# Kernel tuning notes

Hardware: AMD Instinct MI355X
Metric: run time of the kernel (lower is better)

The kernel has to match this reference:

```python
import jax, jax.numpy as jnp
import numpy as np

N_NODES = 50000
N_EDGES = 1600000
NUM_GRAPHS = 64


def gcn_conv(x, edge_index, edge_weight, W, b):
    # PyG GCNConv with normalize=False: h = x @ W; out[i] = sum_{e: tgt(e)=i} w_e * h[src(e)]; out += b
    h = x @ W                                   # [N, out]
    src, tgt = edge_index[0], edge_index[1]
    msg = h[src] * edge_weight[:, None]         # [E, out] gather + scale
    out = jax.ops.segment_sum(msg, tgt, num_segments=N_NODES)
    return out + b


def setup_inputs() -> dict:
    key = jax.random.key(0)
    ks = jax.random.split(key, 10)
    x = jax.random.normal(ks[0], (N_NODES, 128), dtype=jnp.float32)
    edge_index = jax.random.randint(ks[1], (2, N_EDGES), 0, N_NODES, dtype=jnp.int64)
    edge_weight = jax.random.uniform(ks[2], (N_EDGES,), dtype=jnp.float32)
    batch = jnp.sort(jax.random.randint(ks[3], (N_NODES,), 0, NUM_GRAPHS, dtype=jnp.int64))
    W1 = jax.random.normal(ks[4], (128, 64), dtype=jnp.float32) * 0.09  # ~glorot scale
    b1 = jax.random.normal(ks[5], (64,), dtype=jnp.float32) * 0.01
    W2 = jax.random.normal(ks[6], (64, 64), dtype=jnp.float32) * 0.125
    b2 = jax.random.normal(ks[7], (64,), dtype=jnp.float32) * 0.01
    W3 = jax.random.normal(ks[8], (64, 64), dtype=jnp.float32) * 0.125
    b3 = jax.random.normal(ks[9], (64,), dtype=jnp.float32) * 0.01
    return {"x": x, "edge_index": edge_index, "edge_weight": edge_weight, "batch": batch,
            "W1": W1, "b1": b1, "W2": W2, "b2": b2, "W3": W3, "b3": b3}


def reference(x, edge_index, edge_weight, batch, W1, b1, W2, b2, W3, b3):
    # dropout is identity in eval mode
    h = jax.nn.relu(gcn_conv(x, edge_index, edge_weight, W1, b1))
    embed = gcn_conv(h, edge_index, edge_weight, W2, b2)
    graph = gcn_conv(h, edge_index, edge_weight, W3, b3)
    graph_embed = jax.ops.segment_sum(graph, batch, num_segments=NUM_GRAPHS)
    return (embed, graph_embed)
```

## Files before the change

### kernel.cpp

```cpp
#include <hip/hip_runtime.h>


typedef _Float16 f16;
typedef _Float16 h2v __attribute__((ext_vector_type(2)));
typedef _Float16 h4v __attribute__((ext_vector_type(4)));

#define THREADS 256
#define BTHREADS 1024
#define NODECAP 80
#define NC 391
#define CSTRIDE 16
#define ACH 4096
#define CAPC 4736

#define SMEM_BYTES (128 * 68 * 2 + 128 * 64 * 2)

__device__ __forceinline__ void bin_coarse_body(
    int bid, char* smem, const int* __restrict__ src,
    const int* __restrict__ tgt, const float* __restrict__ ew,
    int* __restrict__ cnt_a, int2* __restrict__ cbins, int E) {
  int* lcnt  = (int*)smem;
  int* gbase = lcnt + NC;
  int tid = threadIdx.x;
  for (int i = tid; i < NC; i += THREADS) lcnt[i] = 0;
  __syncthreads();

  int e0 = bid * ACH;
  int xr[16], wr[16], cr[16];
#pragma unroll
  for (int k = 0; k < 16; ++k) {
    int e = e0 + k * THREADS + tid;
    if (e < E) {
      int t = tgt[e];
      int c = t >> 7;
      int r = atomicAdd(&lcnt[c], 1);
      xr[k] = (src[e] & 0xffff) | ((t & 127) << 16);
      wr[k] = __float_as_int(ew[e]);
      cr[k] = c | (r << 16);
    } else {
      cr[k] = -1;
    }
  }
  __syncthreads();

  for (int c = tid; c < NC; c += THREADS) {
    int n = lcnt[c];
    gbase[c] = n ? atomicAdd(&cnt_a[c * CSTRIDE], n) : 0;
  }
  __syncthreads();

#pragma unroll
  for (int k = 0; k < 16; ++k) {
    if (cr[k] < 0) continue;
    int c = cr[k] & 0xffff;
    int r = cr[k] >> 16;
    int dst = gbase[c] + r;
    if (dst < CAPC) cbins[(size_t)c * CAPC + dst] = make_int2(xr[k], wr[k]);
  }
}

__device__ __forceinline__ void gemm1_body(
    int bid, char* smem, const float* __restrict__ A,
    const float* __restrict__ W, f16* __restrict__ C, int M) {
  f16 (*Xs)[68] = (f16(*)[68])smem;
  f16 (*Ws)[64] = (f16(*)[64])(smem + 128 * 68 * 2);
  int tid = threadIdx.x;
  int r0 = bid * 64;

  for (int i = tid * 4; i < 128 * 64; i += THREADS * 4) {
    float4 w = *(const float4*)(W + i);
    h4v p;
    p.x = (f16)w.x; p.y = (f16)w.y; p.z = (f16)w.z; p.w = (f16)w.w;
    *(h4v*)&Ws[0][i] = p;
  }

  for (int i = tid * 4; i < 64 * 128; i += THREADS * 4) {
    int row = i >> 7, k = i & 127;
    float4 v = make_float4(0.f, 0.f, 0.f, 0.f);
    if (r0 + row < M) v = *(const float4*)(A + (size_t)(r0 + row) * 128 + k);
    Xs[k + 0][row] = (f16)v.x; Xs[k + 1][row] = (f16)v.y;
    Xs[k + 2][row] = (f16)v.z; Xs[k + 3][row] = (f16)v.w;
  }
  __syncthreads();

  int tx = tid & 15, ty = tid >> 4;
  float acc[4][4] = {};
#pragma unroll 8
  for (int k = 0; k < 128; ++k) {
    h4v w4 = *(const h4v*)&Ws[k][tx * 4];
    h4v x4 = *(const h4v*)&Xs[k][ty * 4];
    float wx = (float)w4.x, wy = (float)w4.y, wz = (float)w4.z, ww = (float)w4.w;
    float xx = (float)x4.x, xy = (float)x4.y, xz = (float)x4.z, xw = (float)x4.w;
    acc[0][0] = fmaf(xx, wx, acc[0][0]); acc[0][1] = fmaf(xx, wy, acc[0][1]);
    acc[0][2] = fmaf(xx, wz, acc[0][2]); acc[0][3] = fmaf(xx, ww, acc[0][3]);
    acc[1][0] = fmaf(xy, wx, acc[1][0]); acc[1][1] = fmaf(xy, wy, acc[1][1]);
    acc[1][2] = fmaf(xy, wz, acc[1][2]); acc[1][3] = fmaf(xy, ww, acc[1][3]);
    acc[2][0] = fmaf(xz, wx, acc[2][0]); acc[2][1] = fmaf(xz, wy, acc[2][1]);
    acc[2][2] = fmaf(xz, wz, acc[2][2]); acc[2][3] = fmaf(xz, ww, acc[2][3]);
    acc[3][0] = fmaf(xw, wx, acc[3][0]); acc[3][1] = fmaf(xw, wy, acc[3][1]);
    acc[3][2] = fmaf(xw, wz, acc[3][2]); acc[3][3] = fmaf(xw, ww, acc[3][3]);
  }
#pragma unroll
  for (int i = 0; i < 4; ++i) {
    int r = r0 + ty * 4 + i;
    if (r >= M) continue;
    union { f16 h4[4]; uint2 u; } pk;
    pk.h4[0] = (f16)acc[i][0]; pk.h4[1] = (f16)acc[i][1];
    pk.h4[2] = (f16)acc[i][2]; pk.h4[3] = (f16)acc[i][3];
    *(uint2*)(C + (size_t)r * 64 + tx * 4) = pk.u;
  }
}

__global__ __launch_bounds__(THREADS, 4) void k_bin_gemm(
    const int* __restrict__ src, const int* __restrict__ tgt,
    const float* __restrict__ ew, int* __restrict__ cnt_a,
    int2* __restrict__ cbins, int E,
    const float* __restrict__ x, const float* __restrict__ W1,
    f16* __restrict__ hpre, int M, int NBIN, int NGEMM) {
  __shared__ __align__(16) char smem[SMEM_BYTES];
  int b = blockIdx.x;
  int binid = (b % 3 == 0) ? b / 3 : -1;
  if (binid >= 0 && binid < NBIN) {
    bin_coarse_body(binid, smem, src, tgt, ew, cnt_a, cbins, E);
  } else {
    int nb = min((b + 2) / 3, NBIN);
    int gi = b - nb;
    if (gi < NGEMM) gemm1_body(gi, smem, x, W1, hpre, M);
  }
}

__global__ __launch_bounds__(BTHREADS) void bin_fine(
    const int* __restrict__ cnt_a, const int2* __restrict__ cbins,
    int* __restrict__ cnt_f, int2* __restrict__ fbins, int N) {
  __shared__ int fcnt[128];
  int c = blockIdx.x;
  int tid = threadIdx.x;
  if (tid < 128) fcnt[tid] = 0;
  __syncthreads();
  int d = min(cnt_a[c * CSTRIDE], CAPC);
  const int2* ep = cbins + (size_t)c * CAPC;
  for (int i = tid; i < d; i += BTHREADS) {
    int2 ent = ep[i];
    int tl = ent.x >> 16;
    int r = atomicAdd(&fcnt[tl], 1);
    int node = c * 128 + tl;
    if (r < NODECAP && node < N)
      fbins[(size_t)node * NODECAP + r] = make_int2((ent.x & 0xffff) << 7, ent.y);
  }
  __syncthreads();
  if (tid < 128) {
    int node = c * 128 + tid;
    if (node < N) cnt_f[node] = min(fcnt[tid], NODECAP);
  }
}

template <bool RELU>
__global__ __launch_bounds__(THREADS) void gather_nodes(
    const f16* __restrict__ h, const int2* __restrict__ fbins,
    const int* __restrict__ cnt, const float* __restrict__ bias,
    f16* __restrict__ out, int N) {
  int tid = threadIdx.x;
  int lane = tid & 63;
  int node = blockIdx.x * 4 + (tid >> 6);
  if (node >= N) return;
  int d = min(cnt[node], NODECAP);
  const int2* ep = fbins + (size_t)node * NODECAP;
  const char* hb = (const char*)h;
  int q = lane >> 4;
  int lq = lane & 15;
  int lq8 = lq * 8;
  float4 acc = make_float4(0.f, 0.f, 0.f, 0.f);

  for (int base = 0; base < d; base += 64) {
    int take = min(64, d - base);
    int2 ent = ep[base + min(lane, take - 1)];
    int pv = ent.x;
    float wv = (lane < take) ? __int_as_float(ent.y) : 0.f;

    for (int g0 = 0; g0 < take; g0 += 32) {
      int off[8]; float w[8];
#pragma unroll
      for (int u = 0; u < 8; ++u) {
        int sl = g0 + u * 4 + q;
        off[u] = __shfl(pv, sl, 64);
        w[u]   = __shfl(wv, sl, 64);
      }
      uint2 r8[8];
#pragma unroll
      for (int u = 0; u < 8; ++u)
        r8[u] = *(const uint2*)(hb + off[u] + lq8);
#pragma unroll
      for (int u = 0; u < 8; ++u) {
        h2v p0 = __builtin_bit_cast(h2v, r8[u].x);
        h2v p1 = __builtin_bit_cast(h2v, r8[u].y);
        acc.x = fmaf((float)p0.x, w[u], acc.x);
        acc.y = fmaf((float)p0.y, w[u], acc.y);
        acc.z = fmaf((float)p1.x, w[u], acc.z);
        acc.w = fmaf((float)p1.y, w[u], acc.w);
      }
    }
  }

  acc.x += __shfl_xor(acc.x, 16, 64); acc.x += __shfl_xor(acc.x, 32, 64);
  acc.y += __shfl_xor(acc.y, 16, 64); acc.y += __shfl_xor(acc.y, 32, 64);
  acc.z += __shfl_xor(acc.z, 16, 64); acc.z += __shfl_xor(acc.z, 32, 64);
  acc.w += __shfl_xor(acc.w, 16, 64); acc.w += __shfl_xor(acc.w, 32, 64);

  if (q == 0) {
    union { f16 h4[4]; uint2 u; } pk;
    if (RELU) {
      float4 bb = *(const float4*)(bias + lq * 4);
      pk.h4[0] = (f16)fmaxf(acc.x + bb.x, 0.f);
      pk.h4[1] = (f16)fmaxf(acc.y + bb.y, 0.f);
      pk.h4[2] = (f16)fmaxf(acc.z + bb.z, 0.f);
      pk.h4[3] = (f16)fmaxf(acc.w + bb.w, 0.f);
    } else {
      pk.h4[0] = (f16)acc.x; pk.h4[1] = (f16)acc.y;
      pk.h4[2] = (f16)acc.z; pk.h4[3] = (f16)acc.w;
    }
    *(uint2*)((char*)out + (size_t)node * 128 + lq8) = pk.u;
  }
}

__global__ __launch_bounds__(THREADS) void k_gemm2_reduce(
    const f16* __restrict__ A, const float* __restrict__ W,
    const float* __restrict__ bias, const int* __restrict__ batch,
    float* __restrict__ C, float* __restrict__ B, float* __restrict__ counts,
    int M) {
  __shared__ float Xs[64][68];
  __shared__ float Ws[64][64];
  __shared__ int bsh[64];
  int tid = threadIdx.x;
  int r0 = blockIdx.x * 64;

  for (int i = tid * 4; i < 64 * 64; i += THREADS * 4)
    *(float4*)&Ws[0][i] = *(const float4*)(W + i);
  if (tid < 64) bsh[tid] = (r0 + tid < M) ? batch[r0 + tid] : -1;

  for (int i = tid * 4; i < 64 * 64; i += THREADS * 4) {
    int row = i >> 6, k = i & 63;
    float4 v = make_float4(0.f, 0.f, 0.f, 0.f);
    if (r0 + row < M) {
      uint2 u = *(const uint2*)(A + (size_t)(r0 + row) * 64 + k);
      h2v a0 = __builtin_bit_cast(h2v, u.x);
      h2v a1 = __builtin_bit_cast(h2v, u.y);
      v = make_float4((float)a0.x, (float)a0.y, (float)a1.x, (float)a1.y);
    }
    Xs[k + 0][row] = v.x; Xs[k + 1][row] = v.y;
    Xs[k + 2][row] = v.z; Xs[k + 3][row] = v.w;
  }
  __syncthreads();

  int tx = tid & 15, ty = tid >> 4;
  float acc[4][4] = {};
#pragma unroll 8
  for (int k = 0; k < 64; ++k) {
    float4 w4 = *(const float4*)&Ws[k][tx * 4];
    float4 x4 = *(const float4*)&Xs[k][ty * 4];
    acc[0][0] = fmaf(x4.x, w4.x, acc[0][0]); acc[0][1] = fmaf(x4.x, w4.y, acc[0][1]);
    acc[0][2] = fmaf(x4.x, w4.z, acc[0][2]); acc[0][3] = fmaf(x4.x, w4.w, acc[0][3]);
    acc[1][0] = fmaf(x4.y, w4.x, acc[1][0]); acc[1][1] = fmaf(x4.y, w4.y, acc[1][1]);
    acc[1][2] = fmaf(x4.y, w4.z, acc[1][2]); acc[1][3] = fmaf(x4.y, w4.w, acc[1][3]);
    acc[2][0] = fmaf(x4.z, w4.x, acc[2][0]); acc[2][1] = fmaf(x4.z, w4.y, acc[2][1]);
    acc[2][2] = fmaf(x4.z, w4.z, acc[2][2]); acc[2][3] = fmaf(x4.z, w4.w, acc[2][3]);
    acc[3][0] = fmaf(x4.w, w4.x, acc[3][0]); acc[3][1] = fmaf(x4.w, w4.y, acc[3][1]);
    acc[3][2] = fmaf(x4.w, w4.z, acc[3][2]); acc[3][3] = fmaf(x4.w, w4.w, acc[3][3]);
  }
#pragma unroll
  for (int i = 0; i < 4; ++i) {
    int r = r0 + ty * 4 + i;
    if (r >= M) continue;
    float4 bb = *(const float4*)(bias + tx * 4);
    float4 o = make_float4(acc[i][0] + bb.x, acc[i][1] + bb.y,
                           acc[i][2] + bb.z, acc[i][3] + bb.w);
    *(float4*)(C + (size_t)r * 64 + tx * 4) = o;
  }

  int k = tid & 63, p = tid >> 6;
  float racc = 0.f, rcnt = 0.f;
  int cur = -1;
#pragma unroll 4
  for (int j = 0; j < 16; ++j) {
    int row = p * 16 + j;
    if (r0 + row >= M) break;
    int g = bsh[row];
    if (g != cur) {
      if (cur >= 0) {
        unsafeAtomicAdd(&B[cur * 64 + k], racc);
        if (k == 0) unsafeAtomicAdd(&counts[cur], rcnt);
      }
      racc = 0.f; rcnt = 0.f; cur = g;
    }
    racc += Xs[k][row];
    rcnt += 1.f;
  }
  if (cur >= 0) {
    unsafeAtomicAdd(&B[cur * 64 + k], racc);
    if (k == 0) unsafeAtomicAdd(&counts[cur], rcnt);
  }
}

__global__ __launch_bounds__(THREADS) void graph_out_k(
    const float* __restrict__ B, const float* __restrict__ W3,
    const float* __restrict__ b3, const float* __restrict__ counts,
    float* __restrict__ out, int G) {
  int j = threadIdx.x & 63;
  int g = blockIdx.x * (THREADS >> 6) + (threadIdx.x >> 6);
  if (g >= G) return;
  float acc = 0.f;
#pragma unroll
  for (int k = 0; k < 64; ++k) acc += B[g * 64 + k] * W3[k * 64 + j];
  out[g * 64 + j] = acc + counts[g] * b3[j];
}

extern "C" void kernel_launch(void* const* d_in, const int* in_sizes, int n_in,
                              void* d_out, int out_size, void* d_ws, size_t ws_size,
                              hipStream_t stream) {
  const float* x     = (const float*)d_in[0];
  const int*   ei    = (const int*)d_in[1];
  const float* ew    = (const float*)d_in[2];
  const int*   batch = (const int*)d_in[3];
  const float* W1    = (const float*)d_in[4];
  const float* b1    = (const float*)d_in[5];
  const float* W2    = (const float*)d_in[6];
  const float* b2    = (const float*)d_in[7];
  const float* W3    = (const float*)d_in[8];
  const float* b3    = (const float*)d_in[9];

  const int N = in_sizes[0] / 128;
  const int E = in_sizes[1] / 2;
  const int G = (out_size - N * 64) / 64;
  const int* src = ei;
  const int* tgt = ei + E;
  const int NBIN = (E + ACH - 1) / ACH;
  const int NGEMM = (N + 63) / 64;

  float* out_embed = (float*)d_out;
  float* out_graph = (float*)d_out + (size_t)N * 64;

  char* ws = (char*)d_ws;
  f16*   hpre   = (f16*)ws;
  f16*   h1     = hpre + (size_t)N * 64;
  f16*   A      = h1 + (size_t)N * 64;
  int*   cnt_f  = (int*)(A + (size_t)N * 64);
  int*   cnt_a  = cnt_f + N;
  float* B      = (float*)(cnt_a + NC * CSTRIDE);
  float* counts = B + (size_t)G * 64;
  size_t zero_bytes = (size_t)NC * CSTRIDE * 4 + (size_t)(G * 64 + G) * 4;
  size_t off = ((size_t)((char*)(counts + G) - ws) + 255) & ~(size_t)255;
  int2*  fbins  = (int2*)(ws + off);
  off += (size_t)N * NODECAP * 8;
  off = (off + 255) & ~(size_t)255;
  int2*  cbins  = (int2*)(ws + off);

  hipMemsetAsync(cnt_a, 0, zero_bytes, stream);

  k_bin_gemm<<<NBIN + NGEMM, THREADS, 0, stream>>>(
      src, tgt, ew, cnt_a, cbins, E, x, W1, hpre, N, NBIN, NGEMM);

  bin_fine<<<NC, BTHREADS, 0, stream>>>(cnt_a, cbins, cnt_f, fbins, N);

  const int gblocks = (N + 3) / 4;
  gather_nodes<true><<<gblocks, THREADS, 0, stream>>>(
      hpre, fbins, cnt_f, b1, h1, N);
  gather_nodes<false><<<gblocks, THREADS, 0, stream>>>(
      h1, fbins, cnt_f, nullptr, A, N);

  k_gemm2_reduce<<<NGEMM, THREADS, 0, stream>>>(
      A, W2, b2, batch, out_embed, B, counts, N);

  graph_out_k<<<(G + 3) / 4, THREADS, 0, stream>>>(B, W3, b3, counts, out_graph, G);
}
```

Measured before the change: 231.6 us.

## Compact fine edge bins into CSR layout with shared-memory staging

The fine binning pass now counts entries per node, prefix-sums them in shared memory, reserves a contiguous range through a global atomic cursor, stages the entries in LDS and writes them out coalesced as a compact CSR array with per-node start offsets. This replaces the fixed NODECAP-strided padded bins, so the gather kernels read denser edge lists and the writes from bin_fine are contiguous instead of scattered. In exchange bin_fine makes an extra pass over the coarse bins, adds a scan with several barriers, and uses about 38KB of LDS per block. Node order in the fbins array now depends on the order of the atomic cursor.

```diff
diff --git a/kernel.cpp b/kernel.cpp
--- a/kernel.cpp
+++ b/kernel.cpp
@@ -131,40 +131,71 @@
 
 __global__ __launch_bounds__(BTHREADS) void bin_fine(
     const int* __restrict__ cnt_a, const int2* __restrict__ cbins,
-    int* __restrict__ cnt_f, int2* __restrict__ fbins, int N) {
+    int* __restrict__ cursor, int* __restrict__ cnt_f,
+    int* __restrict__ starts, int2* __restrict__ fbins, int N) {
   __shared__ int fcnt[128];
+  __shared__ int pfx[129];
+  __shared__ int2 stg[CAPC];
+  __shared__ int basec;
   int c = blockIdx.x;
   int tid = threadIdx.x;
   if (tid < 128) fcnt[tid] = 0;
   __syncthreads();
   int d = min(cnt_a[c * CSTRIDE], CAPC);
   const int2* ep = cbins + (size_t)c * CAPC;
+
+  for (int i = tid; i < d; i += BTHREADS)
+    atomicAdd(&fcnt[ep[i].x >> 16], 1);
+  __syncthreads();
+
+  if (tid < 128) pfx[tid + 1] = fcnt[tid];
+  if (tid == 0) pfx[0] = 0;
+  __syncthreads();
+#pragma unroll
+  for (int s = 1; s <= 64; s <<= 1) {
+    int v = 0;
+    if (tid < 129 && tid >= s) v = pfx[tid - s];
+    __syncthreads();
+    if (tid < 129 && tid >= s) pfx[tid] += v;
+    __syncthreads();
+  }
+  if (tid == 0) basec = atomicAdd(cursor, pfx[128]);
+  if (tid < 128) fcnt[tid] = 0;
+  __syncthreads();
+
   for (int i = tid; i < d; i += BTHREADS) {
     int2 ent = ep[i];
     int tl = ent.x >> 16;
     int r = atomicAdd(&fcnt[tl], 1);
-    int node = c * 128 + tl;
-    if (r < NODECAP && node < N)
-      fbins[(size_t)node * NODECAP + r] = make_int2((ent.x & 0xffff) << 7, ent.y);
-  }
-  __syncthreads();
+    if (r < NODECAP)
+      stg[pfx[tl] + r] = make_int2((ent.x & 0xffff) << 7, ent.y);
+  }
+  __syncthreads();
+
+  int total = pfx[128];
+  int bc = basec;
+  for (int i = tid; i < total; i += BTHREADS)
+    fbins[(size_t)bc + i] = stg[i];
   if (tid < 128) {
     int node = c * 128 + tid;
-    if (node < N) cnt_f[node] = min(fcnt[tid], NODECAP);
+    if (node < N) {
+      cnt_f[node]  = min(fcnt[tid], NODECAP);
+      starts[node] = bc + pfx[tid];
+    }
   }
 }
 
 template <bool RELU>
 __global__ __launch_bounds__(THREADS) void gather_nodes(
     const f16* __restrict__ h, const int2* __restrict__ fbins,
-    const int* __restrict__ cnt, const float* __restrict__ bias,
-    f16* __restrict__ out, int N) {
+    const int* __restrict__ cnt, const int* __restrict__ starts,
+    const float* __restrict__ bias, f16* __restrict__ out, int N) {
   int tid = threadIdx.x;
   int lane = tid & 63;
   int node = blockIdx.x * 4 + (tid >> 6);
   if (node >= N) return;
-  int d = min(cnt[node], NODECAP);
-  const int2* ep = fbins + (size_t)node * NODECAP;
+  int d = cnt[node];
+  const int2* ep = fbins + starts[node];
   const char* hb = (const char*)h;
   int q = lane >> 4;
   int lq = lane & 15;
@@ -343,13 +374,15 @@
   f16*   h1     = hpre + (size_t)N * 64;
   f16*   A      = h1 + (size_t)N * 64;
   int*   cnt_f  = (int*)(A + (size_t)N * 64);
-  int*   cnt_a  = cnt_f + N;
+  int*   starts = cnt_f + N;
+  int*   cnt_a  = starts + N;
   float* B      = (float*)(cnt_a + NC * CSTRIDE);
   float* counts = B + (size_t)G * 64;
-  size_t zero_bytes = (size_t)NC * CSTRIDE * 4 + (size_t)(G * 64 + G) * 4;
-  size_t off = ((size_t)((char*)(counts + G) - ws) + 255) & ~(size_t)255;
+  int*   cursor = (int*)(counts + G);
+  size_t zero_bytes = (size_t)NC * CSTRIDE * 4 + (size_t)(G * 64 + G) * 4 + 4;
+  size_t off = ((size_t)((char*)(cursor + 1) - ws) + 255) & ~(size_t)255;
   int2*  fbins  = (int2*)(ws + off);
-  off += (size_t)N * NODECAP * 8;
+  off += (size_t)E * 8;
   off = (off + 255) & ~(size_t)255;
   int2*  cbins  = (int2*)(ws + off);
 
@@ -358,13 +391,14 @@
   k_bin_gemm<<<NBIN + NGEMM, THREADS, 0, stream>>>(
       src, tgt, ew, cnt_a, cbins, E, x, W1, hpre, N, NBIN, NGEMM);
 
-  bin_fine<<<NC, BTHREADS, 0, stream>>>(cnt_a, cbins, cnt_f, fbins, N);
+  bin_fine<<<NC, BTHREADS, 0, stream>>>(
+      cnt_a, cbins, cursor, cnt_f, starts, fbins, N);
 
   const int gblocks = (N + 3) / 4;
   gather_nodes<true><<<gblocks, THREADS, 0, stream>>>(
-      hpre, fbins, cnt_f, b1, h1, N);
+      hpre, fbins, cnt_f, starts, b1, h1, N);
   gather_nodes<false><<<gblocks, THREADS, 0, stream>>>(
-      h1, fbins, cnt_f, nullptr, A, N);
+      h1, fbins, cnt_f, starts, nullptr, A, N);
 
   k_gemm2_reduce<<<NGEMM, THREADS, 0, stream>>>(
       A, W2, b2, batch, out_embed, B, counts, N);
```

After: 234.2 us. Within noise of the previous version (+1.1%).

## Stream X rows directly from global in GEMM1, dropping shared-memory X tile

Applied to the files above, without the earlier changes.

The first-layer GEMM no longer stages a transposed f16 copy of the X tile in shared memory. Each thread now reads two X rows straight from global memory as float4 and computes 2x8 outputs against W held in shared memory. This shrinks shared memory use and removes the transposing stores, which lets launch bounds rise to 6 blocks per CU for the fused bin/gemm kernel. In exchange, the X loads become per-thread strided global reads that rely on the cache for coalescing, and there is more register pressure under the tighter launch bound.

```diff
diff --git a/kernel.cpp b/kernel.cpp
--- a/kernel.cpp
+++ b/kernel.cpp
@@ -13,7 +13,7 @@
 #define ACH 4096
 #define CAPC 4736
 
-#define SMEM_BYTES (128 * 68 * 2 + 128 * 64 * 2)
+#define SMEM_BYTES (128 * 64 * 2)
 
 __device__ __forceinline__ void bin_coarse_body(
     int bid, char* smem, const int* __restrict__ src,
@@ -60,10 +60,9 @@
 }
 
 __device__ __forceinline__ void gemm1_body(
-    int bid, char* smem, const float* __restrict__ A,
+    int bid, char* smem, const float* __restrict__ X,
     const float* __restrict__ W, f16* __restrict__ C, int M) {
-  f16 (*Xs)[68] = (f16(*)[68])smem;
-  f16 (*Ws)[64] = (f16(*)[64])(smem + 128 * 68 * 2);
+  f16 (*Ws)[64] = (f16(*)[64])smem;
   int tid = threadIdx.x;
   int r0 = bid * 64;
 
@@ -73,45 +72,48 @@
     p.x = (f16)w.x; p.y = (f16)w.y; p.z = (f16)w.z; p.w = (f16)w.w;
     *(h4v*)&Ws[0][i] = p;
   }
-
-  for (int i = tid * 4; i < 64 * 128; i += THREADS * 4) {
-    int row = i >> 7, k = i & 127;
-    float4 v = make_float4(0.f, 0.f, 0.f, 0.f);
-    if (r0 + row < M) v = *(const float4*)(A + (size_t)(r0 + row) * 128 + k);
-    Xs[k + 0][row] = (f16)v.x; Xs[k + 1][row] = (f16)v.y;
-    Xs[k + 2][row] = (f16)v.z; Xs[k + 3][row] = (f16)v.w;
-  }
-  __syncthreads();
-
-  int tx = tid & 15, ty = tid >> 4;
-  float acc[4][4] = {};
-#pragma unroll 8
-  for (int k = 0; k < 128; ++k) {
-    h4v w4 = *(const h4v*)&Ws[k][tx * 4];
-    h4v x4 = *(const h4v*)&Xs[k][ty * 4];
-    float wx = (float)w4.x, wy = (float)w4.y, wz = (float)w4.z, ww = (float)w4.w;
-    float xx = (float)x4.x, xy = (float)x4.y, xz = (float)x4.z, xw = (float)x4.w;
-    acc[0][0] = fmaf(xx, wx, acc[0][0]); acc[0][1] = fmaf(xx, wy, acc[0][1]);
-    acc[0][2] = fmaf(xx, wz, acc[0][2]); acc[0][3] = fmaf(xx, ww, acc[0][3]);
-    acc[1][0] = fmaf(xy, wx, acc[1][0]); acc[1][1] = fmaf(xy, wy, acc[1][1]);
-    acc[1][2] = fmaf(xy, wz, acc[1][2]); acc[1][3] = fmaf(xy, ww, acc[1][3]);
-    acc[2][0] = fmaf(xz, wx, acc[2][0]); acc[2][1] = fmaf(xz, wy, acc[2][1]);
-    acc[2][2] = fmaf(xz, wz, acc[2][2]); acc[2][3] = fmaf(xz, ww, acc[2][3]);
-    acc[3][0] = fmaf(xw, wx, acc[3][0]); acc[3][1] = fmaf(xw, wy, acc[3][1]);
-    acc[3][2] = fmaf(xw, wz, acc[3][2]); acc[3][3] = fmaf(xw, ww, acc[3][3]);
-  }
-#pragma unroll
-  for (int i = 0; i < 4; ++i) {
-    int r = r0 + ty * 4 + i;
+  __syncthreads();
+
+  int oc = tid & 7;
+  int rp = tid >> 3;
+  int r_a = r0 + rp * 2, r_b = r_a + 1;
+  const float* xa = X + (size_t)r_a * 128;
+  const float* xb = X + (size_t)r_b * 128;
+  bool va = r_a < M, vb = r_b < M;
+  float acc[2][8] = {};
+
+#pragma unroll 2
+  for (int k0 = 0; k0 < 128; k0 += 4) {
+    float4 a4 = va ? *(const float4*)(xa + k0) : make_float4(0.f, 0.f, 0.f, 0.f);
+    float4 b4 = vb ? *(const float4*)(xb + k0) : make_float4(0.f, 0.f, 0.f, 0.f);
+    float ar[4] = {a4.x, a4.y, a4.z, a4.w};
+    float br[4] = {b4.x, b4.y, b4.z, b4.w};
+#pragma unroll
+    for (int jj = 0; jj < 4; ++jj) {
+      h4v w0 = *(const h4v*)&Ws[k0 + jj][oc * 8];
+      h4v w1 = *(const h4v*)&Ws[k0 + jj][oc * 8 + 4];
+      float wf[8] = {(float)w0.x, (float)w0.y, (float)w0.z, (float)w0.w,
+                     (float)w1.x, (float)w1.y, (float)w1.z, (float)w1.w};
+#pragma unroll
+      for (int j = 0; j < 8; ++j) {
+        acc[0][j] = fmaf(ar[jj], wf[j], acc[0][j]);
+        acc[1][j] = fmaf(br[jj], wf[j], acc[1][j]);
+      }
+    }
+  }
+
+#pragma unroll
+  for (int rr = 0; rr < 2; ++rr) {
+    int r = r_a + rr;
     if (r >= M) continue;
-    union { f16 h4[4]; uint2 u; } pk;
-    pk.h4[0] = (f16)acc[i][0]; pk.h4[1] = (f16)acc[i][1];
-    pk.h4[2] = (f16)acc[i][2]; pk.h4[3] = (f16)acc[i][3];
-    *(uint2*)(C + (size_t)r * 64 + tx * 4) = pk.u;
-  }
-}
-
-__global__ __launch_bounds__(THREADS, 4) void k_bin_gemm(
+    union { f16 h8[8]; uint4 u; } pk;
+#pragma unroll
+    for (int j = 0; j < 8; ++j) pk.h8[j] = (f16)acc[rr][j];
+    *(uint4*)(C + (size_t)r * 64 + oc * 8) = pk.u;
+  }
+}
+
+__global__ __launch_bounds__(THREADS, 6) void k_bin_gemm(
     const int* __restrict__ src, const int* __restrict__ tgt,
     const float* __restrict__ ew, int* __restrict__ cnt_a,
     int2* __restrict__ cbins, int E,
```

After: 240.9 us. 1.04x slower.
